# Performance work log

Hardware: AMD Instinct MI355X
Metric: run time of the kernel (lower is better)

The kernel has to match this reference:

```python
import jax, jax.numpy as jnp
import numpy as np

EPS = 1e-10

def _iou(a, b):
    """IoU for boxes in (cx, cy, w, h) format; a, b: (..., 4)."""
    a_min = a[..., :2] - a[..., 2:] * 0.5
    a_max = a[..., :2] + a[..., 2:] * 0.5
    b_min = b[..., :2] - b[..., 2:] * 0.5
    b_max = b[..., :2] + b[..., 2:] * 0.5
    inter_wh = jnp.clip(jnp.minimum(a_max, b_max) - jnp.maximum(a_min, b_min), 0.0)
    inter = inter_wh[..., 0] * inter_wh[..., 1]
    area_a = a[..., 2] * a[..., 3]
    area_b = b[..., 2] * b[..., 3]
    return inter / (area_a + area_b - inter + EPS)

def setup_inputs() -> dict:
    key = jax.random.key(0)
    k1, k2, k3 = jax.random.split(key, 3)
    BATCH, S, C = 16384, 7, 30
    # uniform in (0.01, 1) so sqrt() of w,h channels is finite/differentiable
    preds = jax.random.uniform(k1, (BATCH, S, S, C), jnp.float32, 0.01, 1.0)
    labels = jax.random.uniform(k2, (BATCH, S, S, C), jnp.float32, 0.01, 1.0)
    obj = jax.random.bernoulli(k3, 0.15, (BATCH, S, S)).astype(jnp.float32)
    labels = labels.at[..., 4].set(obj)  # code branches on labels[...,4] == 1
    return {"preds": preds, "labels": labels}

def reference(preds, labels):
    batch = preds.shape[0]
    obj = labels[..., 4] == 1.0  # (B, S, S)
    # faithful quirk: label bbox x-coord is read transposed (labels[i, y, x, 0])
    lb0 = jnp.swapaxes(labels[..., 0], 1, 2)
    lbox = jnp.stack([lb0, labels[..., 1], labels[..., 2], labels[..., 3]], axis=-1)
    iou1 = _iou(preds[..., 0:4], lbox)
    iou2 = _iou(preds[..., 5:9], lbox)
    choose1 = iou1 > iou2
    # branch where box 1 is responsible
    b1 = (5.0 * jnp.sum((preds[..., 0:2] - labels[..., 0:2]) ** 2, -1)
          + jnp.sum((jnp.sqrt(preds[..., 2:4]) - jnp.sqrt(labels[..., 2:4])) ** 2, -1)
          + (iou1 - preds[..., 4]) ** 2
          + 0.5 * preds[..., 9] ** 2)
    # branch where box 2 is responsible (targets read from labels[...,5:9] as in source)
    b2 = (5.0 * jnp.sum((preds[..., 5:7] - labels[..., 5:7]) ** 2, -1)
          + jnp.sum((jnp.sqrt(preds[..., 7:9]) - jnp.sqrt(labels[..., 7:9])) ** 2, -1)
          + (iou2 - preds[..., 9]) ** 2
          + 0.5 * preds[..., 4] ** 2)
    cls = jnp.sum((labels[..., 10:] - preds[..., 10:]) ** 2, -1)
    obj_loss = jnp.where(choose1, b1, b2) + cls
    noobj_loss = 0.5 * (preds[..., 4] ** 2 + preds[..., 9] ** 2)
    total = jnp.sum(jnp.where(obj, obj_loss, noobj_loss))
    return total / batch
```

## Files before the change

### kernel.cpp

```cpp
#include <hip/hip_runtime.h>


#define BATCH 16384
#define S 7
#define C 30
#define NCELLS (BATCH * S * S)
#define BLOCK 256
#define NC 256
#define NGRP (NCELLS / NC)
#define NBLK2 (NGRP / 2)

typedef float f4v __attribute__((ext_vector_type(4)));

__device__ __forceinline__ f4v ntld(const f4v* p) {
    return __builtin_nontemporal_load(p);
}

__device__ __forceinline__ float sq(float v) { return v * v; }

__device__ __forceinline__ float iou_box(float acx, float acy, float aw, float ah,
                                         float bcx, float bcy, float bw, float bh) {
    float ax0 = acx - aw * 0.5f, ax1 = acx + aw * 0.5f;
    float ay0 = acy - ah * 0.5f, ay1 = acy + ah * 0.5f;
    float bx0 = bcx - bw * 0.5f, bx1 = bcx + bw * 0.5f;
    float by0 = bcy - bh * 0.5f, by1 = bcy + bh * 0.5f;
    float iw = fmaxf(fminf(ax1, bx1) - fmaxf(ax0, bx0), 0.0f);
    float ih = fmaxf(fminf(ay1, by1) - fmaxf(ay0, by0), 0.0f);
    float inter = iw * ih;
    float denom = aw * ah + bw * bh - inter + 1e-10f;
    return inter / denom;
}

__device__ __forceinline__ void stage_regs(const float* __restrict__ preds,
                                           const float* __restrict__ labels,
                                           int base_cell, int tid, int tl,
                                           f4v* rp, f4v* rl) {
    const f4v* gp = reinterpret_cast<const f4v*>(preds  + (size_t)base_cell * C);
    const f4v* gl = reinterpret_cast<const f4v*>(labels + (size_t)base_cell * C);
    #pragma unroll
    for (int k = 0; k < 7; ++k) rl[k] = ntld(gl + tid + k * BLOCK);
    #pragma unroll
    for (int k = 0; k < 7; ++k) rp[k] = ntld(gp + tid + k * BLOCK);
    if (tid < 128) rl[7] = ntld(gl + tl);
    else           rp[7] = ntld(gp + tl);
}

__device__ __forceinline__ void write_lds(float* sp, float* sl, int tid, int tl,
                                          const f4v* rp, const f4v* rl) {
    f4v* s4l = reinterpret_cast<f4v*>(sl);
    f4v* s4p = reinterpret_cast<f4v*>(sp);
    #pragma unroll
    for (int k = 0; k < 7; ++k) s4l[tid + k * BLOCK] = rl[k];
    #pragma unroll
    for (int k = 0; k < 7; ++k) s4p[tid + k * BLOCK] = rp[k];
    if (tid < 128) s4l[tl] = rl[7];
    else           s4p[tl] = rp[7];
}

__device__ __forceinline__ float cell_loss(const float* __restrict__ sp,
                                           const float* __restrict__ sl,
                                           const float* __restrict__ labels,
                                           int base_cell, int tid) {
    const float* p = sp + tid * C;
    const float* l = sl + tid * C;
    float pv[C], lv[C];
    #pragma unroll
    for (int i = 0; i < C / 2; ++i) {
        float2 tp = *reinterpret_cast<const float2*>(p + 2 * i);
        pv[2 * i] = tp.x; pv[2 * i + 1] = tp.y;
        float2 tl2 = *reinterpret_cast<const float2*>(l + 2 * i);
        lv[2 * i] = tl2.x; lv[2 * i + 1] = tl2.y;
    }

    int cell = base_cell + tid;
    int b    = cell / (S * S);
    int rem  = cell - b * (S * S);
    int y    = rem / S;
    int x    = rem - y * S;
    int pc   = b * (S * S) + x * S + y;
    float lb0;
    if (pc >= base_cell && pc < base_cell + NC) {
        lb0 = sl[(pc - base_cell) * C];
    } else {
        lb0 = labels[(size_t)pc * C];
    }

    float iou1 = iou_box(pv[0], pv[1], pv[2], pv[3], lb0, lv[1], lv[2], lv[3]);
    float iou2 = iou_box(pv[5], pv[6], pv[7], pv[8], lb0, lv[1], lv[2], lv[3]);

    float b1 = 5.0f * (sq(pv[0] - lv[0]) + sq(pv[1] - lv[1]))
             + sq(sqrtf(pv[2]) - sqrtf(lv[2])) + sq(sqrtf(pv[3]) - sqrtf(lv[3]))
             + sq(iou1 - pv[4])
             + 0.5f * pv[9] * pv[9];

    float b2 = 5.0f * (sq(pv[5] - lv[5]) + sq(pv[6] - lv[6]))
             + sq(sqrtf(pv[7]) - sqrtf(lv[7])) + sq(sqrtf(pv[8]) - sqrtf(lv[8]))
             + sq(iou2 - pv[9])
             + 0.5f * pv[4] * pv[4];

    float cls = 0.0f;
    #pragma unroll
    for (int c = 10; c < C; ++c) cls += sq(lv[c] - pv[c]);

    float obj_loss   = ((iou1 > iou2) ? b1 : b2) + cls;
    float noobj_loss = 0.5f * (pv[4] * pv[4] + pv[9] * pv[9]);
    return (lv[4] == 1.0f) ? obj_loss : noobj_loss;
}

__global__ __launch_bounds__(BLOCK) void yolo_partial_kernel(
        const float* __restrict__ preds,
        const float* __restrict__ labels,
        float* __restrict__ partials) {
    __shared__ __align__(16) float sp[NC * C];
    __shared__ __align__(16) float sl[NC * C];
    __shared__ float wsum[BLOCK / 64];

    const int tid  = threadIdx.x;
    const int lane = tid & 63;
    const int wv   = tid >> 6;
    const int tl   = 1792 + (tid & 127);
    const int g0   = blockIdx.x * 2;
    const int g1   = g0 + 1;

    f4v rl[8], rp[8];

    stage_regs(preds, labels, g0 * NC, tid, tl, rp, rl);
    write_lds(sp, sl, tid, tl, rp, rl);
    __syncthreads();

    stage_regs(preds, labels, g1 * NC, tid, tl, rp, rl);

    float loss = cell_loss(sp, sl, labels, g0 * NC, tid);
    #pragma unroll
    for (int off = 32; off > 0; off >>= 1)
        loss += __shfl_down(loss, off, 64);
    if (lane == 0) wsum[wv] = loss;
    __syncthreads();
    if (tid == 0)
        partials[g0] = wsum[0] + wsum[1] + wsum[2] + wsum[3];

    write_lds(sp, sl, tid, tl, rp, rl);
    __syncthreads();

    loss = cell_loss(sp, sl, labels, g1 * NC, tid);
    #pragma unroll
    for (int off = 32; off > 0; off >>= 1)
        loss += __shfl_down(loss, off, 64);
    if (lane == 0) wsum[wv] = loss;
    __syncthreads();
    if (tid == 0)
        partials[g1] = wsum[0] + wsum[1] + wsum[2] + wsum[3];
}

__global__ __launch_bounds__(BLOCK) void yolo_reduce_kernel(
        const float* __restrict__ partials,
        float* __restrict__ out) {
    const int tid = threadIdx.x;
    float s = 0.0f;
    for (int i = tid; i < NGRP; i += BLOCK) s += partials[i];

    #pragma unroll
    for (int off = 32; off > 0; off >>= 1)
        s += __shfl_down(s, off, 64);

    __shared__ float wsum[BLOCK / 64];
    int lane = tid & 63;
    int wv   = tid >> 6;
    if (lane == 0) wsum[wv] = s;
    __syncthreads();
    if (tid == 0) {
        out[0] = (wsum[0] + wsum[1] + wsum[2] + wsum[3]) * (1.0f / (float)BATCH);
    }
}

extern "C" void kernel_launch(void* const* d_in, const int* in_sizes, int n_in,
                              void* d_out, int out_size, void* d_ws, size_t ws_size,
                              hipStream_t stream) {
    const float* preds  = (const float*)d_in[0];
    const float* labels = (const float*)d_in[1];
    float* out = (float*)d_out;
    float* partials = (float*)d_ws;

    yolo_partial_kernel<<<NBLK2, BLOCK, 0, stream>>>(preds, labels, partials);
    yolo_reduce_kernel<<<1, BLOCK, 0, stream>>>(partials, out);
}
```

Baseline: 198.6 us.

## Halve block size and process each group as two sequential half-tiles

Blocks shrink to 128 threads, and each block handles one 256-cell group as two 128-cell halves staged through a half-size LDS buffer. This cuts shared memory per block so more blocks can be resident per CU. In exchange, the previous software prefetch of the next group during compute is removed, and the transposed label lookup has a smaller LDS window, so more of those reads go to global memory.

```diff
diff --git a/kernel.cpp b/kernel.cpp
--- a/kernel.cpp
+++ b/kernel.cpp
@@ -5,10 +5,11 @@
 #define S 7
 #define C 30
 #define NCELLS (BATCH * S * S)
-#define BLOCK 256
+#define BLOCK 128
 #define NC 256
+#define HALF 128
 #define NGRP (NCELLS / NC)
-#define NBLK2 (NGRP / 2)
+#define F4_PER_HALF (HALF * C / 4)
 
 typedef float f4v __attribute__((ext_vector_type(4)));
 
@@ -33,19 +34,19 @@
 
 __device__ __forceinline__ void stage_regs(const float* __restrict__ preds,
                                            const float* __restrict__ labels,
-                                           int base_cell, int tid, int tl,
+                                           int hbase, int tid,
                                            f4v* rp, f4v* rl) {
-    const f4v* gp = reinterpret_cast<const f4v*>(preds  + (size_t)base_cell * C);
-    const f4v* gl = reinterpret_cast<const f4v*>(labels + (size_t)base_cell * C);
+    const f4v* gp = reinterpret_cast<const f4v*>(preds  + (size_t)hbase * C);
+    const f4v* gl = reinterpret_cast<const f4v*>(labels + (size_t)hbase * C);
     #pragma unroll
     for (int k = 0; k < 7; ++k) rl[k] = ntld(gl + tid + k * BLOCK);
     #pragma unroll
     for (int k = 0; k < 7; ++k) rp[k] = ntld(gp + tid + k * BLOCK);
-    if (tid < 128) rl[7] = ntld(gl + tl);
-    else           rp[7] = ntld(gp + tl);
+    if (tid < 64) rl[7] = ntld(gl + 896 + tid);
+    else          rp[7] = ntld(gp + 896 + (tid - 64));
 }
 
-__device__ __forceinline__ void write_lds(float* sp, float* sl, int tid, int tl,
+__device__ __forceinline__ void write_lds(float* sp, float* sl, int tid,
                                           const f4v* rp, const f4v* rl) {
     f4v* s4l = reinterpret_cast<f4v*>(sl);
     f4v* s4p = reinterpret_cast<f4v*>(sp);
@@ -53,14 +54,14 @@
     for (int k = 0; k < 7; ++k) s4l[tid + k * BLOCK] = rl[k];
     #pragma unroll
     for (int k = 0; k < 7; ++k) s4p[tid + k * BLOCK] = rp[k];
-    if (tid < 128) s4l[tl] = rl[7];
-    else           s4p[tl] = rp[7];
+    if (tid < 64) s4l[896 + tid] = rl[7];
+    else          s4p[896 + (tid - 64)] = rp[7];
 }
 
 __device__ __forceinline__ float cell_loss(const float* __restrict__ sp,
                                            const float* __restrict__ sl,
                                            const float* __restrict__ labels,
-                                           int base_cell, int tid) {
+                                           int hbase, int tid) {
     const float* p = sp + tid * C;
     const float* l = sl + tid * C;
     float pv[C], lv[C];
@@ -72,15 +73,15 @@
         lv[2 * i] = tl2.x; lv[2 * i + 1] = tl2.y;
     }
 
-    int cell = base_cell + tid;
+    int cell = hbase + tid;
     int b    = cell / (S * S);
     int rem  = cell - b * (S * S);
     int y    = rem / S;
     int x    = rem - y * S;
     int pc   = b * (S * S) + x * S + y;
     float lb0;
-    if (pc >= base_cell && pc < base_cell + NC) {
-        lb0 = sl[(pc - base_cell) * C];
+    if (pc >= hbase && pc < hbase + HALF) {
+        lb0 = sl[(pc - hbase) * C];
     } else {
         lb0 = labels[(size_t)pc * C];
     }
@@ -111,59 +112,58 @@
         const float* __restrict__ preds,
         const float* __restrict__ labels,
         float* __restrict__ partials) {
-    __shared__ __align__(16) float sp[NC * C];
-    __shared__ __align__(16) float sl[NC * C];
-    __shared__ float wsum[BLOCK / 64];
+    __shared__ __align__(16) float sp[HALF * C];
+    __shared__ __align__(16) float sl[HALF * C];
+    __shared__ float wsA[2], wsB[2];
 
     const int tid  = threadIdx.x;
     const int lane = tid & 63;
     const int wv   = tid >> 6;
-    const int tl   = 1792 + (tid & 127);
-    const int g0   = blockIdx.x * 2;
-    const int g1   = g0 + 1;
+    const int g    = blockIdx.x;
+    const int hA   = g * NC;
+    const int hB   = hA + HALF;
 
     f4v rl[8], rp[8];
 
-    stage_regs(preds, labels, g0 * NC, tid, tl, rp, rl);
-    write_lds(sp, sl, tid, tl, rp, rl);
+    stage_regs(preds, labels, hA, tid, rp, rl);
+    write_lds(sp, sl, tid, rp, rl);
     __syncthreads();
 
-    stage_regs(preds, labels, g1 * NC, tid, tl, rp, rl);
-
-    float loss = cell_loss(sp, sl, labels, g0 * NC, tid);
+    float loss = cell_loss(sp, sl, labels, hA, tid);
     #pragma unroll
     for (int off = 32; off > 0; off >>= 1)
         loss += __shfl_down(loss, off, 64);
-    if (lane == 0) wsum[wv] = loss;
-    __syncthreads();
-    if (tid == 0)
-        partials[g0] = wsum[0] + wsum[1] + wsum[2] + wsum[3];
-
-    write_lds(sp, sl, tid, tl, rp, rl);
+    if (lane == 0) wsA[wv] = loss;
     __syncthreads();
 
-    loss = cell_loss(sp, sl, labels, g1 * NC, tid);
+    stage_regs(preds, labels, hB, tid, rp, rl);
+    write_lds(sp, sl, tid, rp, rl);
+    __syncthreads();
+
+    loss = cell_loss(sp, sl, labels, hB, tid);
     #pragma unroll
     for (int off = 32; off > 0; off >>= 1)
         loss += __shfl_down(loss, off, 64);
-    if (lane == 0) wsum[wv] = loss;
+    if (lane == 0) wsB[wv] = loss;
     __syncthreads();
-    if (tid == 0)
-        partials[g1] = wsum[0] + wsum[1] + wsum[2] + wsum[3];
+
+    if (tid == 0) {
+        partials[g] = ((wsA[0] + wsA[1]) + wsB[0]) + wsB[1];
+    }
 }
 
-__global__ __launch_bounds__(BLOCK) void yolo_reduce_kernel(
+__global__ __launch_bounds__(256) void yolo_reduce_kernel(
         const float* __restrict__ partials,
         float* __restrict__ out) {
     const int tid = threadIdx.x;
     float s = 0.0f;
-    for (int i = tid; i < NGRP; i += BLOCK) s += partials[i];
+    for (int i = tid; i < NGRP; i += 256) s += partials[i];
 
     #pragma unroll
     for (int off = 32; off > 0; off >>= 1)
         s += __shfl_down(s, off, 64);
 
-    __shared__ float wsum[BLOCK / 64];
+    __shared__ float wsum[4];
     int lane = tid & 63;
     int wv   = tid >> 6;
     if (lane == 0) wsum[wv] = s;
@@ -181,6 +181,6 @@
     float* out = (float*)d_out;
     float* partials = (float*)d_ws;
 
-    yolo_partial_kernel<<<NBLK2, BLOCK, 0, stream>>>(preds, labels, partials);
-    yolo_reduce_kernel<<<1, BLOCK, 0, stream>>>(partials, out);
+    yolo_partial_kernel<<<NGRP, BLOCK, 0, stream>>>(preds, labels, partials);
+    yolo_reduce_kernel<<<1, 256, 0, stream>>>(partials, out);
 }
```

Result: no change. 199.1 us (+0.2%).
